# Optimization experiments

Measured on AMD Instinct MI355X. Metric: run time of the kernel, lower is better.

## Reference

```python
import jax, jax.numpy as jnp
import numpy as np
import math

B, N, T, F_IN, F_OUT = 8, 512, 12, 32, 64


def setup_inputs() -> dict:
    key = jax.random.key(0)
    k1, k2, k3, k4, k5 = jax.random.split(key, 5)
    x = jax.random.normal(k1, (B, N, T, F_IN), dtype=jnp.float32)
    phaseAct_matrix = jax.random.uniform(k2, (B, T, N, N), dtype=jnp.float32)
    adj = jax.random.uniform(k3, (N, N), dtype=jnp.float32)  # sym-normalized adjacency stand-in
    mask = (jax.random.uniform(k4, (N,)) < 0.5).astype(jnp.float32)  # 1 = observed node, 0 = unknown
    theta = jax.random.normal(k5, (F_IN, F_OUT), dtype=jnp.float32) * 0.05
    return {"x": x, "phaseAct_matrix": phaseAct_matrix, "adj": adj, "mask": mask, "theta": theta}


def _spatial_attention(x):
    # x: (B, N, T, F) -> scores (B, T, N, N)
    f = x.shape[-1]
    xt = x.transpose(0, 2, 1, 3)  # (B, T, N, F)
    score = jnp.einsum('btnf,btmf->btnm', xt, xt) / math.sqrt(f)
    return jax.nn.softmax(score, axis=-1)


def reference(x, phaseAct_matrix, adj, mask, theta):
    f = x.shape[-1]
    t_steps = x.shape[2]
    inv_sqrt_f = 1.0 / math.sqrt(f)
    m = mask[None, :, None, None]  # broadcast over (B, N, T-1, F)

    def body(i, x_cur):
        sa = _spatial_attention(x_cur) * inv_sqrt_f          # (B, T, N, N)
        sat_act = (phaseAct_matrix * sa).transpose(0, 1, 3, 2)  # (B, T, N, N) transposed
        xt = x_cur.transpose(0, 2, 1, 3)                     # (B, T, N, F)
        # predict step t from step t-1: (B, T-1, N, F)
        x_pred = jnp.einsum('btnm,btmf->btnf', sat_act[:, 1:], xt[:, :t_steps - 1])
        x_pred = x_pred.transpose(0, 2, 1, 3)                # (B, N, T-1, F)
        # revise_unknown: keep observed nodes, impute unknown nodes at steps 1..T-1
        x_rev = x_cur[:, :, 1:, :] * m + x_pred * (1.0 - m)
        return jnp.concatenate([x_cur[:, :, 0:1, :], x_rev], axis=2)

    x = jax.lax.fori_loop(1, t_steps, body, x)

    sa = _spatial_attention(x) * inv_sqrt_f                  # (B, T, N, N)
    satAct_adj = phaseAct_matrix * adj[None, None] * sa      # (B, T, N, N)
    xt = x.transpose(0, 2, 1, 3)                             # (B, T, N, F)
    agg = jnp.einsum('btmn,btmf->btnf', satAct_adj, xt)      # transpose(adj) @ x
    out = jax.nn.relu(jnp.einsum('btnf,fo->btno', agg, theta))  # (B, T, N, F_out)
    return out.transpose(0, 2, 1, 3)                         # (B, N, T, F_out)
```

## Files before the change

kernel.cpp:

```cpp
#include <hip/hip_runtime.h>


#define B_ 8
#define N_ 512
#define T_ 12
#define F_ 32
#define O_ 64
#define MT 1
#define NW 8

typedef unsigned int uint_t;
typedef unsigned short ushort_t;
typedef _Float16 f16_t;
typedef _Float16 f16x4 __attribute__((ext_vector_type(4)));
typedef _Float16 f16x8 __attribute__((ext_vector_type(8)));
typedef float f32x4 __attribute__((ext_vector_type(4)));

__device__ __forceinline__ int xidx(int b, int n, int t, int f) {
    return ((b * N_ + n) * T_ + t) * F_ + f;
}
__device__ __forceinline__ f16x8 load_frag8(const float* p) {
    float4 a = *reinterpret_cast<const float4*>(p);
    float4 b = *reinterpret_cast<const float4*>(p + 4);
    f16x8 r;
    r[0] = (f16_t)a.x; r[1] = (f16_t)a.y; r[2] = (f16_t)a.z; r[3] = (f16_t)a.w;
    r[4] = (f16_t)b.x; r[5] = (f16_t)b.y; r[6] = (f16_t)b.z; r[7] = (f16_t)b.w;
    return r;
}
union U2H4 { uint2 u; f16x4 h; };

__global__ __launch_bounds__(256)
void permute_kernel(const float* __restrict__ src, ushort_t* __restrict__ dst)
{
    __shared__ float Lp[16][516];
    const int tid = threadIdx.x;
    const int mc  = blockIdx.x;
    const int s   = blockIdx.y;
    src += (size_t)s * N_ * N_ + (size_t)mc * 16 * N_;
    uint_t* dstu = (uint_t*)dst + (size_t)s * 131072 + (size_t)mc * 4096;

    #pragma unroll
    for (int k = 0; k < 32; ++k) {
        int idx = tid + 256 * k;
        Lp[idx >> 9][idx & 511] = src[idx];
    }
    __syncthreads();
    #pragma unroll
    for (int k = 0; k < 16; ++k) {
        int u    = tid + 256 * k;
        int nt   = u >> 7;
        int r    = u & 127;
        int quad = r >> 5;
        int cl   = (r >> 1) & 15;
        int m0   = quad * 4 + (r & 1) * 2;
        int n    = nt * 16 + cl;
        union { f16_t h[2]; uint_t i; } pk;
        pk.h[0] = (f16_t)Lp[m0][n];
        pk.h[1] = (f16_t)Lp[m0 + 1][n];
        dstu[u] = pk.i;
    }
}

template <int FINAL>
__global__ __launch_bounds__(512)
void gcn_kernel(const float* __restrict__ x0,
                const float* __restrict__ xcur,
                float* __restrict__ dst,
                const ushort_t* __restrict__ phase_h,
                const ushort_t* __restrict__ adj_h,
                const float* __restrict__ mask)
{
    __shared__ float2 st[2][NW][16];

    const int tid  = threadIdx.x;
    const int w    = tid >> 6;
    const int l    = tid & 63;
    const int quad = l >> 4;
    const int col  = l & 15;
    const int t    = FINAL ? blockIdx.y : blockIdx.y + 1;
    const int b    = blockIdx.z;
    const int nt0  = w * 4;
    const float inv_f = 0.17677669529663687f;

    const float* xs     = (FINAL && t == 0) ? x0 : xcur;
    const float* xp_src = FINAL ? xs : ((t == 1) ? x0 : xcur);
    const int    tp     = FINAL ? t : t - 1;

    f16x8 bf[4];
    #pragma unroll
    for (int i = 0; i < 4; ++i)
        bf[i] = load_frag8(&xs[xidx(b, (nt0 + i) * 16 + col, t, quad * 8)]);

    f32x4 acc[4][2];
    #pragma unroll
    for (int i = 0; i < 4; ++i) {
        acc[i][0] = (f32x4){0.f, 0.f, 0.f, 0.f};
        acc[i][1] = (f32x4){0.f, 0.f, 0.f, 0.f};
    }

    const uint_t* phu = (const uint_t*)phase_h + (size_t)(b * T_ + t) * 131072;
    const uint_t* adu = (const uint_t*)adj_h;

    for (int c = 0; c < 512 / (MT * 16); ++c) {
        const int mb = c * 16;
        const int mc = c;

        f16x8 af = load_frag8(&xs[xidx(b, mb + col, t, quad * 8)]);

        U2H4 ph[4], aj[4];
        #pragma unroll
        for (int i = 0; i < 4; ++i) {
            ph[i].u = *(const uint2*)(phu + (size_t)mc * 4096 + (nt0 + i) * 128 + l * 2);
            if (FINAL)
                aj[i].u = *(const uint2*)(adu + (size_t)mc * 4096 + (nt0 + i) * 128 + l * 2);
        }
        f16x4 bp[2];
        #pragma unroll
        for (int ft = 0; ft < 2; ++ft)
            #pragma unroll
            for (int j = 0; j < 4; ++j)
                bp[ft][j] = (f16_t)xp_src[xidx(b, mb + quad * 4 + j, tp, ft * 16 + col)];

        f32x4 s4[4];
        #pragma unroll
        for (int i = 0; i < 4; ++i) {
            s4[i] = __builtin_amdgcn_mfma_f32_16x16x32_f16(
                        af, bf[i], (f32x4){0.f, 0.f, 0.f, 0.f}, 0, 0, 0);
        }
        float mxw[4], sw[4], e[4][4];
        #pragma unroll
        for (int v = 0; v < 4; ++v) {
            #pragma unroll
            for (int i = 0; i < 4; ++i) s4[i][v] *= inv_f;
            mxw[v] = fmaxf(fmaxf(s4[0][v], s4[1][v]), fmaxf(s4[2][v], s4[3][v]));
        }
        #pragma unroll
        for (int d = 1; d < 16; d <<= 1)
            #pragma unroll
            for (int v = 0; v < 4; ++v)
                mxw[v] = fmaxf(mxw[v], __shfl_xor(mxw[v], d, 64));
        #pragma unroll
        for (int v = 0; v < 4; ++v) {
            #pragma unroll
            for (int i = 0; i < 4; ++i) e[i][v] = __expf(s4[i][v] - mxw[v]);
            sw[v] = (e[0][v] + e[1][v]) + (e[2][v] + e[3][v]);
        }
        #pragma unroll
        for (int d = 1; d < 16; d <<= 1)
            #pragma unroll
            for (int v = 0; v < 4; ++v)
                sw[v] += __shfl_xor(sw[v], d, 64);

        const int buf = c & 1;
        if (col < 4) {
            float mv = (col == 0) ? mxw[0] : (col == 1) ? mxw[1] : (col == 2) ? mxw[2] : mxw[3];
            float sv = (col == 0) ? sw[0]  : (col == 1) ? sw[1]  : (col == 2) ? sw[2]  : sw[3];
            st[buf][w][quad * 4 + col] = make_float2(mv, sv);
        }
        __syncthreads();
        {
            const int row = l >> 2, wp = l & 3;
            float2 p0 = st[buf][2 * wp][row];
            float2 p1 = st[buf][2 * wp + 1][row];
            float M = fmaxf(p0.x, p1.x);
            float S = p0.y * __expf(p0.x - M) + p1.y * __expf(p1.x - M);
            #pragma unroll
            for (int d = 1; d < 4; d <<= 1) {
                float Mo = __shfl_xor(M, d, 64), So = __shfl_xor(S, d, 64);
                float Mn = fmaxf(M, Mo);
                S = S * __expf(M - Mn) + So * __expf(Mo - Mn);
                M = Mn;
            }
            #pragma unroll
            for (int v = 0; v < 4; ++v) {
                float Mr = __shfl(M, quad * 16 + v * 4, 64);
                float Sr = __shfl(S, quad * 16 + v * 4, 64);
                mxw[v] = __expf(mxw[v] - Mr) * inv_f / Sr;
            }
        }

        #pragma unroll
        for (int i = 0; i < 4; ++i) {
            f16x4 wf;
            if (FINAL) {
                #pragma unroll
                for (int v = 0; v < 4; ++v)
                    wf[v] = (f16_t)(e[i][v] * mxw[v] * (float)ph[i].h[v] * (float)aj[i].h[v]);
            } else {
                #pragma unroll
                for (int v = 0; v < 4; ++v)
                    wf[v] = (f16_t)(e[i][v] * mxw[v] * (float)ph[i].h[v]);
            }
            #pragma unroll
            for (int ft = 0; ft < 2; ++ft)
                acc[i][ft] = __builtin_amdgcn_mfma_f32_16x16x16f16(wf, bp[ft], acc[i][ft], 0, 0, 0);
        }
    }

    #pragma unroll
    for (int i = 0; i < 4; ++i) {
        #pragma unroll
        for (int v = 0; v < 4; ++v) {
            const int n = (nt0 + i) * 16 + quad * 4 + v;
            if (FINAL) {
                float* d0 = &dst[((b * T_ + t) * N_ + n) * F_ + col];
                d0[0]  = acc[i][0][v];
                d0[16] = acc[i][1][v];
            } else {
                const int i0 = xidx(b, n, t, col);
                const float mk  = mask[n];
                const float xc0 = xcur[i0];
                const float xc1 = xcur[i0 + 16];
                dst[i0]      = (mk != 0.f) ? xc0 : acc[i][0][v];
                dst[i0 + 16] = (mk != 0.f) ? xc1 : acc[i][1][v];
            }
        }
    }
}

__global__ __launch_bounds__(256)
void proj_kernel(const float* __restrict__ agg, const float* __restrict__ theta,
                 float* __restrict__ out)
{
    __shared__ float th[F_ * O_];
    int tid = threadIdx.x;
    #pragma unroll
    for (int p = 0; p < 8; ++p) th[tid + 256 * p] = theta[tid + 256 * p];
    __syncthreads();
    int g  = blockIdx.x * 256 + tid;
    int o  = g & 63;
    int r  = g >> 6;
    int tt = r % T_;
    int r2 = r / T_;
    int n  = r2 & 511;
    int b  = r2 >> 9;
    const float* a = &agg[((b * T_ + tt) * N_ + n) * F_];
    float s = 0.f;
    #pragma unroll
    for (int f = 0; f < F_; ++f) s += a[f] * th[f * O_ + o];
    out[g] = fmaxf(s, 0.f);
}

extern "C" void kernel_launch(void* const* d_in, const int* in_sizes, int n_in,
                              void* d_out, int out_size, void* d_ws, size_t ws_size,
                              hipStream_t stream)
{
    const float* x     = (const float*)d_in[0];
    const float* phase = (const float*)d_in[1];
    const float* adj   = (const float*)d_in[2];
    const float* mask  = (const float*)d_in[3];
    const float* theta = (const float*)d_in[4];
    float* out = (float*)d_out;

    const size_t XE = (size_t)B_ * N_ * T_ * F_;
    float*    xA      = (float*)d_ws;
    float*    xB      = xA + XE;
    float*    agg     = xB + XE;
    ushort_t* phase_h = (ushort_t*)(agg + XE);
    ushort_t* adj_h   = phase_h + (size_t)96 * N_ * N_;

    permute_kernel<<<dim3(32, 96), 256, 0, stream>>>(phase, phase_h);
    permute_kernel<<<dim3(32, 1), 256, 0, stream>>>(adj, adj_h);

    const float* cur = x;
    float* bufs[2] = { xA, xB };
    for (int i = 0; i < T_ - 1; ++i) {
        float* nxt = bufs[i & 1];
        gcn_kernel<0><<<dim3(1, T_ - 1, B_), 512, 0, stream>>>(
            x, cur, nxt, phase_h, adj_h, mask);
        cur = nxt;
    }
    gcn_kernel<1><<<dim3(1, T_, B_), 512, 0, stream>>>(
        x, cur, agg, phase_h, adj_h, mask);
    proj_kernel<<<(B_ * N_ * T_ * O_) / 256, 256, 0, stream>>>(agg, theta, out);
}
```

Before: 1.061 ms.

## Split softmax into stats pass and weighted pass, double block to 1024 threads

The fused loop used to do a block-wide barrier every 16-row chunk to combine per-wave softmax max and sum. It now runs a first pass that writes per-wave row statistics to shared memory, merges them once after a single barrier, and then runs a second pass that recomputes the scores and exponentials with the final max and normaliser. Each block now has 16 waves, each handling 2 column tiles instead of 4, so there are more waves per block even though the grid stays small. The cost is computing the score MFMAs and exponentials twice, plus more shared memory.

```diff
diff --git a/kernel.cpp b/kernel.cpp
--- a/kernel.cpp
+++ b/kernel.cpp
@@ -6,8 +6,7 @@
 #define T_ 12
 #define F_ 32
 #define O_ 64
-#define MT 1
-#define NW 8
+#define NW 16
 
 typedef unsigned int uint_t;
 typedef unsigned short ushort_t;
@@ -62,7 +61,7 @@
 }
 
 template <int FINAL>
-__global__ __launch_bounds__(512)
+__global__ __launch_bounds__(1024)
 void gcn_kernel(const float* __restrict__ x0,
                 const float* __restrict__ xcur,
                 float* __restrict__ dst,
@@ -70,7 +69,8 @@
                 const ushort_t* __restrict__ adj_h,
                 const float* __restrict__ mask)
 {
-    __shared__ float2 st[2][NW][16];
+    __shared__ float2 stw[NW][N_];
+    __shared__ float2 MSl[N_];
 
     const int tid  = threadIdx.x;
     const int w    = tid >> 6;
@@ -79,37 +79,90 @@
     const int col  = l & 15;
     const int t    = FINAL ? blockIdx.y : blockIdx.y + 1;
     const int b    = blockIdx.z;
-    const int nt0  = w * 4;
+    const int nt0  = w * 2;
     const float inv_f = 0.17677669529663687f;
 
     const float* xs     = (FINAL && t == 0) ? x0 : xcur;
     const float* xp_src = FINAL ? xs : ((t == 1) ? x0 : xcur);
     const int    tp     = FINAL ? t : t - 1;
 
-    f16x8 bf[4];
-    #pragma unroll
-    for (int i = 0; i < 4; ++i)
+    f16x8 bf[2];
+    #pragma unroll
+    for (int i = 0; i < 2; ++i)
         bf[i] = load_frag8(&xs[xidx(b, (nt0 + i) * 16 + col, t, quad * 8)]);
 
-    f32x4 acc[4][2];
-    #pragma unroll
-    for (int i = 0; i < 4; ++i) {
+    const uint_t* phu = (const uint_t*)phase_h + (size_t)(b * T_ + t) * 131072;
+    const uint_t* adu = (const uint_t*)adj_h;
+
+    #pragma unroll 2
+    for (int c = 0; c < 32; ++c) {
+        const int mb = c * 16;
+        f16x8 af = load_frag8(&xs[xidx(b, mb + col, t, quad * 8)]);
+
+        f32x4 s4[2];
+        #pragma unroll
+        for (int i = 0; i < 2; ++i)
+            s4[i] = __builtin_amdgcn_mfma_f32_16x16x32_f16(
+                        af, bf[i], (f32x4){0.f, 0.f, 0.f, 0.f}, 0, 0, 0);
+
+        float mxw[4], sw[4];
+        #pragma unroll
+        for (int v = 0; v < 4; ++v) {
+            s4[0][v] *= inv_f; s4[1][v] *= inv_f;
+            mxw[v] = fmaxf(s4[0][v], s4[1][v]);
+        }
+        #pragma unroll
+        for (int d = 1; d < 16; d <<= 1)
+            #pragma unroll
+            for (int v = 0; v < 4; ++v)
+                mxw[v] = fmaxf(mxw[v], __shfl_xor(mxw[v], d, 64));
+        #pragma unroll
+        for (int v = 0; v < 4; ++v)
+            sw[v] = __expf(s4[0][v] - mxw[v]) + __expf(s4[1][v] - mxw[v]);
+        #pragma unroll
+        for (int d = 1; d < 16; d <<= 1)
+            #pragma unroll
+            for (int v = 0; v < 4; ++v)
+                sw[v] += __shfl_xor(sw[v], d, 64);
+
+        if (col < 4) {
+            float mv = (col == 0) ? mxw[0] : (col == 1) ? mxw[1] : (col == 2) ? mxw[2] : mxw[3];
+            float sv = (col == 0) ? sw[0]  : (col == 1) ? sw[1]  : (col == 2) ? sw[2]  : sw[3];
+            stw[w][mb + quad * 4 + col] = make_float2(mv, sv);
+        }
+    }
+
+    __syncthreads();
+    if (tid < N_) {
+        float2 p = stw[0][tid];
+        float M = p.x, S = p.y;
+        #pragma unroll
+        for (int ww = 1; ww < NW; ++ww) {
+            p = stw[ww][tid];
+            float Mn = fmaxf(M, p.x);
+            S = S * __expf(M - Mn) + p.y * __expf(p.x - Mn);
+            M = Mn;
+        }
+        MSl[tid] = make_float2(M, inv_f / S);
+    }
+    __syncthreads();
+
+    f32x4 acc[2][2];
+    #pragma unroll
+    for (int i = 0; i < 2; ++i) {
         acc[i][0] = (f32x4){0.f, 0.f, 0.f, 0.f};
         acc[i][1] = (f32x4){0.f, 0.f, 0.f, 0.f};
     }
 
-    const uint_t* phu = (const uint_t*)phase_h + (size_t)(b * T_ + t) * 131072;
-    const uint_t* adu = (const uint_t*)adj_h;
-
-    for (int c = 0; c < 512 / (MT * 16); ++c) {
+    #pragma unroll 2
+    for (int c = 0; c < 32; ++c) {
         const int mb = c * 16;
         const int mc = c;
 
         f16x8 af = load_frag8(&xs[xidx(b, mb + col, t, quad * 8)]);
-
-        U2H4 ph[4], aj[4];
-        #pragma unroll
-        for (int i = 0; i < 4; ++i) {
+        U2H4 ph[2], aj[2];
+        #pragma unroll
+        for (int i = 0; i < 2; ++i) {
             ph[i].u = *(const uint2*)(phu + (size_t)mc * 4096 + (nt0 + i) * 128 + l * 2);
             if (FINAL)
                 aj[i].u = *(const uint2*)(adu + (size_t)mc * 4096 + (nt0 + i) * 128 + l * 2);
@@ -121,75 +174,29 @@
             for (int j = 0; j < 4; ++j)
                 bp[ft][j] = (f16_t)xp_src[xidx(b, mb + quad * 4 + j, tp, ft * 16 + col)];
 
-        f32x4 s4[4];
-        #pragma unroll
-        for (int i = 0; i < 4; ++i) {
+        f32x4 s4[2];
+        #pragma unroll
+        for (int i = 0; i < 2; ++i)
             s4[i] = __builtin_amdgcn_mfma_f32_16x16x32_f16(
                         af, bf[i], (f32x4){0.f, 0.f, 0.f, 0.f}, 0, 0, 0);
-        }
-        float mxw[4], sw[4], e[4][4];
-        #pragma unroll
-        for (int v = 0; v < 4; ++v) {
-            #pragma unroll
-            for (int i = 0; i < 4; ++i) s4[i][v] *= inv_f;
-            mxw[v] = fmaxf(fmaxf(s4[0][v], s4[1][v]), fmaxf(s4[2][v], s4[3][v]));
-        }
-        #pragma unroll
-        for (int d = 1; d < 16; d <<= 1)
-            #pragma unroll
-            for (int v = 0; v < 4; ++v)
-                mxw[v] = fmaxf(mxw[v], __shfl_xor(mxw[v], d, 64));
-        #pragma unroll
-        for (int v = 0; v < 4; ++v) {
-            #pragma unroll
-            for (int i = 0; i < 4; ++i) e[i][v] = __expf(s4[i][v] - mxw[v]);
-            sw[v] = (e[0][v] + e[1][v]) + (e[2][v] + e[3][v]);
-        }
-        #pragma unroll
-        for (int d = 1; d < 16; d <<= 1)
-            #pragma unroll
-            for (int v = 0; v < 4; ++v)
-                sw[v] += __shfl_xor(sw[v], d, 64);
-
-        const int buf = c & 1;
-        if (col < 4) {
-            float mv = (col == 0) ? mxw[0] : (col == 1) ? mxw[1] : (col == 2) ? mxw[2] : mxw[3];
-            float sv = (col == 0) ? sw[0]  : (col == 1) ? sw[1]  : (col == 2) ? sw[2]  : sw[3];
-            st[buf][w][quad * 4 + col] = make_float2(mv, sv);
-        }
-        __syncthreads();
-        {
-            const int row = l >> 2, wp = l & 3;
-            float2 p0 = st[buf][2 * wp][row];
-            float2 p1 = st[buf][2 * wp + 1][row];
-            float M = fmaxf(p0.x, p1.x);
-            float S = p0.y * __expf(p0.x - M) + p1.y * __expf(p1.x - M);
-            #pragma unroll
-            for (int d = 1; d < 4; d <<= 1) {
-                float Mo = __shfl_xor(M, d, 64), So = __shfl_xor(S, d, 64);
-                float Mn = fmaxf(M, Mo);
-                S = S * __expf(M - Mn) + So * __expf(Mo - Mn);
-                M = Mn;
-            }
-            #pragma unroll
-            for (int v = 0; v < 4; ++v) {
-                float Mr = __shfl(M, quad * 16 + v * 4, 64);
-                float Sr = __shfl(S, quad * 16 + v * 4, 64);
-                mxw[v] = __expf(mxw[v] - Mr) * inv_f / Sr;
-            }
-        }
-
-        #pragma unroll
-        for (int i = 0; i < 4; ++i) {
+
+        float2 ms[4];
+        #pragma unroll
+        for (int v = 0; v < 4; ++v) ms[v] = MSl[mb + quad * 4 + v];
+
+        #pragma unroll
+        for (int i = 0; i < 2; ++i) {
             f16x4 wf;
             if (FINAL) {
                 #pragma unroll
                 for (int v = 0; v < 4; ++v)
-                    wf[v] = (f16_t)(e[i][v] * mxw[v] * (float)ph[i].h[v] * (float)aj[i].h[v]);
+                    wf[v] = (f16_t)(__expf(s4[i][v] * inv_f - ms[v].x) * ms[v].y
+                                    * (float)ph[i].h[v] * (float)aj[i].h[v]);
             } else {
                 #pragma unroll
                 for (int v = 0; v < 4; ++v)
-                    wf[v] = (f16_t)(e[i][v] * mxw[v] * (float)ph[i].h[v]);
+                    wf[v] = (f16_t)(__expf(s4[i][v] * inv_f - ms[v].x) * ms[v].y
+                                    * (float)ph[i].h[v]);
             }
             #pragma unroll
             for (int ft = 0; ft < 2; ++ft)
@@ -198,7 +205,7 @@
     }
 
     #pragma unroll
-    for (int i = 0; i < 4; ++i) {
+    for (int i = 0; i < 2; ++i) {
         #pragma unroll
         for (int v = 0; v < 4; ++v) {
             const int n = (nt0 + i) * 16 + quad * 4 + v;
@@ -266,11 +273,11 @@
     float* bufs[2] = { xA, xB };
     for (int i = 0; i < T_ - 1; ++i) {
         float* nxt = bufs[i & 1];
-        gcn_kernel<0><<<dim3(1, T_ - 1, B_), 512, 0, stream>>>(
+        gcn_kernel<0><<<dim3(1, T_ - 1, B_), 1024, 0, stream>>>(
             x, cur, nxt, phase_h, adj_h, mask);
         cur = nxt;
     }
-    gcn_kernel<1><<<dim3(1, T_, B_), 512, 0, stream>>>(
+    gcn_kernel<1><<<dim3(1, T_, B_), 1024, 0, stream>>>(
         x, cur, agg, phase_h, adj_h, mask);
     proj_kernel<<<(B_ * N_ * T_ * O_) / 256, 256, 0, stream>>>(agg, theta, out);
 }
```

Result: slower. 1.386 ms (+30.6%).

## Split softmax stats into separate kernel to parallelize GCN over node tiles

Applied to the files above, without the earlier changes.

Replaces the single-block-per-(b,t) fused kernel with two kernels. The first computes per-column softmax max and normalizer statistics over all nodes. The second uses the precomputed stats to build attention weights per node tile and run the aggregation MFMAs. This removes the per-chunk block-wide cross-wave reduction and __syncthreads, and launches 8x more blocks to fill the GPU. The cost is recomputing the score MFMAs twice, an extra launch per iteration, and a round trip through global memory for the stats.

```diff
diff --git a/kernel.cpp b/kernel.cpp
--- a/kernel.cpp
+++ b/kernel.cpp
@@ -6,8 +6,6 @@
 #define T_ 12
 #define F_ 32
 #define O_ 64
-#define MT 1
-#define NW 8
 
 typedef unsigned int uint_t;
 typedef unsigned short ushort_t;
@@ -62,16 +60,11 @@
 }
 
 template <int FINAL>
-__global__ __launch_bounds__(512)
-void gcn_kernel(const float* __restrict__ x0,
-                const float* __restrict__ xcur,
-                float* __restrict__ dst,
-                const ushort_t* __restrict__ phase_h,
-                const ushort_t* __restrict__ adj_h,
-                const float* __restrict__ mask)
-{
-    __shared__ float2 st[2][NW][16];
-
+__global__ __launch_bounds__(256)
+void stats_kernel(const float* __restrict__ x0,
+                  const float* __restrict__ xcur,
+                  float2* __restrict__ MS)
+{
     const int tid  = threadIdx.x;
     const int w    = tid >> 6;
     const int l    = tid & 63;
@@ -79,141 +72,113 @@
     const int col  = l & 15;
     const int t    = FINAL ? blockIdx.y : blockIdx.y + 1;
     const int b    = blockIdx.z;
-    const int nt0  = w * 4;
+    const int mb   = (blockIdx.x * 4 + w) * 16;
+    const float inv_f = 0.17677669529663687f;
+    const float* xs = (FINAL && t == 0) ? x0 : xcur;
+
+    f16x8 bm = load_frag8(&xs[xidx(b, mb + col, t, quad * 8)]);
+
+    float M = -1e30f, S = 0.f;
+    #pragma unroll 4
+    for (int nt = 0; nt < 32; ++nt) {
+        f16x8 an = load_frag8(&xs[xidx(b, nt * 16 + col, t, quad * 8)]);
+        f32x4 s4 = __builtin_amdgcn_mfma_f32_16x16x32_f16(
+                       an, bm, (f32x4){0.f, 0.f, 0.f, 0.f}, 0, 0, 0);
+        float m4 = fmaxf(fmaxf(s4[0], s4[1]), fmaxf(s4[2], s4[3])) * inv_f;
+        float Mn = fmaxf(M, m4);
+        S = S * __expf(M - Mn)
+          + (__expf(s4[0] * inv_f - Mn) + __expf(s4[1] * inv_f - Mn))
+          + (__expf(s4[2] * inv_f - Mn) + __expf(s4[3] * inv_f - Mn));
+        M = Mn;
+    }
+    #pragma unroll
+    for (int d = 16; d < 64; d <<= 1) {
+        float Mo = __shfl_xor(M, d, 64), So = __shfl_xor(S, d, 64);
+        float Mn = fmaxf(M, Mo);
+        S = S * __expf(M - Mn) + So * __expf(Mo - Mn);
+        M = Mn;
+    }
+    if (l < 16)
+        MS[(size_t)(b * T_ + t) * N_ + mb + l] = make_float2(M, inv_f / S);
+}
+
+template <int FINAL>
+__global__ __launch_bounds__(256)
+void pred_kernel(const float* __restrict__ x0,
+                 const float* __restrict__ xcur,
+                 float* __restrict__ dst,
+                 const ushort_t* __restrict__ phase_h,
+                 const ushort_t* __restrict__ adj_h,
+                 const float* __restrict__ mask,
+                 const float2* __restrict__ MS)
+{
+    const int tid  = threadIdx.x;
+    const int w    = tid >> 6;
+    const int l    = tid & 63;
+    const int quad = l >> 4;
+    const int col  = l & 15;
+    const int t    = FINAL ? blockIdx.y : blockIdx.y + 1;
+    const int b    = blockIdx.z;
+    const int nt   = blockIdx.x * 4 + w;
     const float inv_f = 0.17677669529663687f;
 
     const float* xs     = (FINAL && t == 0) ? x0 : xcur;
     const float* xp_src = FINAL ? xs : ((t == 1) ? x0 : xcur);
     const int    tp     = FINAL ? t : t - 1;
 
-    f16x8 bf[4];
-    #pragma unroll
-    for (int i = 0; i < 4; ++i)
-        bf[i] = load_frag8(&xs[xidx(b, (nt0 + i) * 16 + col, t, quad * 8)]);
-
-    f32x4 acc[4][2];
-    #pragma unroll
-    for (int i = 0; i < 4; ++i) {
-        acc[i][0] = (f32x4){0.f, 0.f, 0.f, 0.f};
-        acc[i][1] = (f32x4){0.f, 0.f, 0.f, 0.f};
-    }
-
-    const uint_t* phu = (const uint_t*)phase_h + (size_t)(b * T_ + t) * 131072;
-    const uint_t* adu = (const uint_t*)adj_h;
-
-    for (int c = 0; c < 512 / (MT * 16); ++c) {
+    f16x8 bf = load_frag8(&xs[xidx(b, nt * 16 + col, t, quad * 8)]);
+    const uint_t* phu = (const uint_t*)phase_h + (size_t)(b * T_ + t) * 131072
+                        + nt * 128 + l * 2;
+    const uint_t* adu = (const uint_t*)adj_h + nt * 128 + l * 2;
+    const float2* msp = MS + (size_t)(b * T_ + t) * N_ + quad * 4;
+
+    f32x4 acc0 = (f32x4){0.f, 0.f, 0.f, 0.f};
+    f32x4 acc1 = (f32x4){0.f, 0.f, 0.f, 0.f};
+
+    #pragma unroll 2
+    for (int c = 0; c < 32; ++c) {
         const int mb = c * 16;
-        const int mc = c;
-
         f16x8 af = load_frag8(&xs[xidx(b, mb + col, t, quad * 8)]);
-
-        U2H4 ph[4], aj[4];
+        U2H4 ph; ph.u = *(const uint2*)(phu + (size_t)c * 4096);
+        U2H4 aj;
+        if (FINAL) aj.u = *(const uint2*)(adu + (size_t)c * 4096);
+        float4 msA = *(const float4*)(msp + mb);
+        float4 msB = *(const float4*)(msp + mb + 2);
+        f16x4 bp0, bp1;
         #pragma unroll
-        for (int i = 0; i < 4; ++i) {
-            ph[i].u = *(const uint2*)(phu + (size_t)mc * 4096 + (nt0 + i) * 128 + l * 2);
-            if (FINAL)
-                aj[i].u = *(const uint2*)(adu + (size_t)mc * 4096 + (nt0 + i) * 128 + l * 2);
+        for (int j = 0; j < 4; ++j) {
+            bp0[j] = (f16_t)xp_src[xidx(b, mb + quad * 4 + j, tp, col)];
+            bp1[j] = (f16_t)xp_src[xidx(b, mb + quad * 4 + j, tp, 16 + col)];
         }
-        f16x4 bp[2];
-        #pragma unroll
-        for (int ft = 0; ft < 2; ++ft)
-            #pragma unroll
-            for (int j = 0; j < 4; ++j)
-                bp[ft][j] = (f16_t)xp_src[xidx(b, mb + quad * 4 + j, tp, ft * 16 + col)];
-
-        f32x4 s4[4];
-        #pragma unroll
-        for (int i = 0; i < 4; ++i) {
-            s4[i] = __builtin_amdgcn_mfma_f32_16x16x32_f16(
-                        af, bf[i], (f32x4){0.f, 0.f, 0.f, 0.f}, 0, 0, 0);
-        }
-        float mxw[4], sw[4], e[4][4];
+
+        f32x4 s4 = __builtin_amdgcn_mfma_f32_16x16x32_f16(
+                       af, bf, (f32x4){0.f, 0.f, 0.f, 0.f}, 0, 0, 0);
+
+        const float Mv[4] = {msA.x, msA.z, msB.x, msB.z};
+        const float Sv[4] = {msA.y, msA.w, msB.y, msB.w};
+        f16x4 wf;
         #pragma unroll
         for (int v = 0; v < 4; ++v) {
-            #pragma unroll
-            for (int i = 0; i < 4; ++i) s4[i][v] *= inv_f;
-            mxw[v] = fmaxf(fmaxf(s4[0][v], s4[1][v]), fmaxf(s4[2][v], s4[3][v]));
+            float e = __expf(s4[v] * inv_f - Mv[v]) * Sv[v] * (float)ph.h[v];
+            if (FINAL) e *= (float)aj.h[v];
+            wf[v] = (f16_t)e;
         }
-        #pragma unroll
-        for (int d = 1; d < 16; d <<= 1)
-            #pragma unroll
-            for (int v = 0; v < 4; ++v)
-                mxw[v] = fmaxf(mxw[v], __shfl_xor(mxw[v], d, 64));
-        #pragma unroll
-        for (int v = 0; v < 4; ++v) {
-            #pragma unroll
-            for (int i = 0; i < 4; ++i) e[i][v] = __expf(s4[i][v] - mxw[v]);
-            sw[v] = (e[0][v] + e[1][v]) + (e[2][v] + e[3][v]);
-        }
-        #pragma unroll
-        for (int d = 1; d < 16; d <<= 1)
-            #pragma unroll
-            for (int v = 0; v < 4; ++v)
-                sw[v] += __shfl_xor(sw[v], d, 64);
-
-        const int buf = c & 1;
-        if (col < 4) {
-            float mv = (col == 0) ? mxw[0] : (col == 1) ? mxw[1] : (col == 2) ? mxw[2] : mxw[3];
-            float sv = (col == 0) ? sw[0]  : (col == 1) ? sw[1]  : (col == 2) ? sw[2]  : sw[3];
-            st[buf][w][quad * 4 + col] = make_float2(mv, sv);
-        }
-        __syncthreads();
-        {
-            const int row = l >> 2, wp = l & 3;
-            float2 p0 = st[buf][2 * wp][row];
-            float2 p1 = st[buf][2 * wp + 1][row];
-            float M = fmaxf(p0.x, p1.x);
-            float S = p0.y * __expf(p0.x - M) + p1.y * __expf(p1.x - M);
-            #pragma unroll
-            for (int d = 1; d < 4; d <<= 1) {
-                float Mo = __shfl_xor(M, d, 64), So = __shfl_xor(S, d, 64);
-                float Mn = fmaxf(M, Mo);
-                S = S * __expf(M - Mn) + So * __expf(Mo - Mn);
-                M = Mn;
-            }
-            #pragma unroll
-            for (int v = 0; v < 4; ++v) {
-                float Mr = __shfl(M, quad * 16 + v * 4, 64);
-                float Sr = __shfl(S, quad * 16 + v * 4, 64);
-                mxw[v] = __expf(mxw[v] - Mr) * inv_f / Sr;
-            }
-        }
-
-        #pragma unroll
-        for (int i = 0; i < 4; ++i) {
-            f16x4 wf;
-            if (FINAL) {
-                #pragma unroll
-                for (int v = 0; v < 4; ++v)
-                    wf[v] = (f16_t)(e[i][v] * mxw[v] * (float)ph[i].h[v] * (float)aj[i].h[v]);
-            } else {
-                #pragma unroll
-                for (int v = 0; v < 4; ++v)
-                    wf[v] = (f16_t)(e[i][v] * mxw[v] * (float)ph[i].h[v]);
-            }
-            #pragma unroll
-            for (int ft = 0; ft < 2; ++ft)
-                acc[i][ft] = __builtin_amdgcn_mfma_f32_16x16x16f16(wf, bp[ft], acc[i][ft], 0, 0, 0);
-        }
-    }
-
-    #pragma unroll
-    for (int i = 0; i < 4; ++i) {
-        #pragma unroll
-        for (int v = 0; v < 4; ++v) {
-            const int n = (nt0 + i) * 16 + quad * 4 + v;
-            if (FINAL) {
-                float* d0 = &dst[((b * T_ + t) * N_ + n) * F_ + col];
-                d0[0]  = acc[i][0][v];
-                d0[16] = acc[i][1][v];
-            } else {
-                const int i0 = xidx(b, n, t, col);
-                const float mk  = mask[n];
-                const float xc0 = xcur[i0];
-                const float xc1 = xcur[i0 + 16];
-                dst[i0]      = (mk != 0.f) ? xc0 : acc[i][0][v];
-                dst[i0 + 16] = (mk != 0.f) ? xc1 : acc[i][1][v];
-            }
+        acc0 = __builtin_amdgcn_mfma_f32_16x16x16f16(wf, bp0, acc0, 0, 0, 0);
+        acc1 = __builtin_amdgcn_mfma_f32_16x16x16f16(wf, bp1, acc1, 0, 0, 0);
+    }
+
+    #pragma unroll
+    for (int v = 0; v < 4; ++v) {
+        const int n = nt * 16 + quad * 4 + v;
+        if (FINAL) {
+            float* d0 = &dst[((size_t)(b * T_ + t) * N_ + n) * F_ + col];
+            d0[0]  = acc0[v];
+            d0[16] = acc1[v];
+        } else {
+            const int i0 = xidx(b, n, t, col);
+            const float mk = mask[n];
+            dst[i0]      = (mk != 0.f) ? xcur[i0]      : acc0[v];
+            dst[i0 + 16] = (mk != 0.f) ? xcur[i0 + 16] : acc1[v];
         }
     }
 }
@@ -258,6 +223,7 @@
     float*    agg     = xB + XE;
     ushort_t* phase_h = (ushort_t*)(agg + XE);
     ushort_t* adj_h   = phase_h + (size_t)96 * N_ * N_;
+    float2*   MS      = (float2*)(adj_h + (size_t)N_ * N_);
 
     permute_kernel<<<dim3(32, 96), 256, 0, stream>>>(phase, phase_h);
     permute_kernel<<<dim3(32, 1), 256, 0, stream>>>(adj, adj_h);
@@ -266,11 +232,13 @@
     float* bufs[2] = { xA, xB };
     for (int i = 0; i < T_ - 1; ++i) {
         float* nxt = bufs[i & 1];
-        gcn_kernel<0><<<dim3(1, T_ - 1, B_), 512, 0, stream>>>(
-            x, cur, nxt, phase_h, adj_h, mask);
+        stats_kernel<0><<<dim3(8, T_ - 1, B_), 256, 0, stream>>>(x, cur, MS);
+        pred_kernel<0><<<dim3(8, T_ - 1, B_), 256, 0, stream>>>(
+            x, cur, nxt, phase_h, adj_h, mask, MS);
         cur = nxt;
     }
-    gcn_kernel<1><<<dim3(1, T_, B_), 512, 0, stream>>>(
-        x, cur, agg, phase_h, adj_h, mask);
+    stats_kernel<1><<<dim3(8, T_, B_), 256, 0, stream>>>(x, cur, MS);
+    pred_kernel<1><<<dim3(8, T_, B_), 256, 0, stream>>>(
+        x, cur, agg, phase_h, adj_h, mask, MS);
     proj_kernel<<<(B_ * N_ * T_ * O_) / 256, 256, 0, stream>>>(agg, theta, out);
 }
```

After: 957.6 us. 1.11x faster.
